# Kernel optimization log

Hardware: AMD Instinct MI355X
Metric: run time of the kernel (lower is better)

## Reference

```python
import jax, jax.numpy as jnp
import numpy as np

B, N, S, C1, C2 = 8, 8192, 2048, 128, 256
H1, H2 = 256, 256
EPS_LN = 1e-5


def _layernorm_c(x, g, b):
    # LayerNorm over channel dim of [B, C, N]
    mu = jnp.mean(x, axis=1, keepdims=True)
    var = jnp.mean((x - mu) ** 2, axis=1, keepdims=True)
    return g[None, :, None] * (x - mu) / jnp.sqrt(var + EPS_LN) + b[None, :, None]


def setup_inputs() -> dict:
    key = jax.random.key(0)
    ks = jax.random.split(key, 8)
    Cin = C1 + C2
    return {
        "points_coor1": jax.random.normal(ks[0], (B, 3, N), jnp.float32),
        "points_coor2": jax.random.normal(ks[1], (B, 3, S), jnp.float32),
        "points_fea1": jax.random.normal(ks[2], (B, C1, N), jnp.float32),
        "points_fea2": jax.random.normal(ks[3], (B, C2, S), jnp.float32),
        "points_padding2": jnp.zeros((B, S), dtype=bool),
        "W1": jax.random.normal(ks[4], (H1, Cin), jnp.float32) * 0.05,
        "b1": jnp.zeros((H1,), jnp.float32),
        "g1": jnp.ones((H1,), jnp.float32),
        "be1": jnp.zeros((H1,), jnp.float32),
        "W2": jax.random.normal(ks[5], (H2, H1), jnp.float32) * 0.05,
        "b2": jnp.zeros((H2,), jnp.float32),
        "g2": jnp.ones((H2,), jnp.float32),
        "be2": jnp.zeros((H2,), jnp.float32),
    }


def reference(points_coor1, points_coor2, points_fea1, points_fea2,
              points_padding2, W1, b1, g1, be1, W2, b2, g2, be2):
    c1 = jnp.transpose(points_coor1, (0, 2, 1))  # [B,N,3]
    c2 = jnp.transpose(points_coor2, (0, 2, 1))  # [B,S,3]
    f2 = jnp.transpose(points_fea2, (0, 2, 1))   # [B,S,C2]

    # push padded points far away (max computed on unmodified coords, as in torch RHS-first eval)
    big = jnp.max(jnp.abs(c2)) * 3.0
    c2 = jnp.where(points_padding2[..., None], big, c2)

    # squared euclidean pairwise distances [B,N,S]
    d = (jnp.sum(c1 * c1, -1)[:, :, None]
         + jnp.sum(c2 * c2, -1)[:, None, :]
         - 2.0 * jnp.einsum('bnd,bsd->bns', c1, c2))

    neg_d, idx = jax.lax.top_k(-d, 3)          # 3 smallest distances
    dists = -neg_d                              # [B,N,3]
    recip = 1.0 / jnp.clip(dists, 1e-8)
    w = recip / jnp.sum(recip, axis=-1, keepdims=True)  # [B,N,3]

    gathered = jax.vmap(lambda f, i: f[i])(f2, idx)     # [B,N,3,C2]
    interp = jnp.einsum('bnkc,bnk->bcn', gathered, w)   # [B,C2,N]

    x = jnp.concatenate([points_fea1, interp], axis=1)  # [B,C1+C2,N]
    x = jax.nn.relu(_layernorm_c(jnp.einsum('oc,bcn->bon', W1, x) + b1[None, :, None], g1, be1))
    x = jax.nn.relu(_layernorm_c(jnp.einsum('oc,bcn->bon', W2, x) + b2[None, :, None], g2, be2))
    return x
```

## Files before the change

### kernel.cpp

```cpp
#include <hip/hip_runtime.h>
#include <stdint.h>

#define BB 8
#define NPT 8192
#define SPT 2048
#define C1D 128
#define C2D 256
#define CIN 384
#define HD 256
#define SPLIT 8
#define SC (SPT/SPLIT)

typedef __attribute__((ext_vector_type(8))) short bf16x8;
typedef __attribute__((ext_vector_type(4))) float f32x4;

#define B2F(u) __uint_as_float(((unsigned int)(u)) << 16)

__device__ __forceinline__ unsigned short f2b(float f){
  unsigned int u = __float_as_uint(f);
  u += 0x7fffu + ((u >> 16) & 1u);
  return (unsigned short)(u >> 16);
}

__device__ __forceinline__ void bar_sync(){
  __builtin_amdgcn_sched_barrier(0);
  asm volatile("s_waitcnt lgkmcnt(0)" ::: "memory");
  __builtin_amdgcn_s_barrier();
  __builtin_amdgcn_sched_barrier(0);
}

__global__ __launch_bounds__(256) void gsrc_kernel(const float* __restrict__ coor2,
    const unsigned char* __restrict__ pad, float4* __restrict__ gs){
  int i = blockIdx.x * 256 + threadIdx.x;
  int b = i >> 11, s = i & (SPT - 1);
  const float* cb = coor2 + b * 3 * SPT;
  float x = cb[s], y = cb[SPT + s], z = cb[2*SPT + s];
  if (pad[i]) { x = 1e19f; y = 1e19f; z = 1e19f; }
  float n2 = __fadd_rn(__fadd_rn(__fmul_rn(x,x), __fmul_rn(y,y)), __fmul_rn(z,z));
  gs[i] = make_float4(x, y, z, n2);
}

#define NB_KNN 2048
#define NB_CVT 640
#define NB_T2 4096
#define NB_T1 8192
__global__ __launch_bounds__(256) void main_kernel(
    const float* __restrict__ coor1, const float4* __restrict__ gs,
    float* __restrict__ cv, int* __restrict__ cj,
    const float* __restrict__ W1, const float* __restrict__ W2, unsigned short* __restrict__ Wb,
    const float* __restrict__ fea2, unsigned short* __restrict__ f2t,
    const float* __restrict__ fea1, unsigned short* __restrict__ xpm){
  __shared__ unsigned short t[32][33];
  int bid = blockIdx.x, tid = threadIdx.x;
  if (bid < NB_KNN){
    int x = bid & 31, b = (bid >> 5) & 7, c = bid >> 8;
    int s0c = c * SC;
    const float4* gsb = gs + b * SPT + s0c;
    int n = x * 256 + tid;
    const float* ca = coor1 + b * 3 * NPT;
    float x1 = ca[n], y1 = ca[NPT + n], z1 = ca[2*NPT + n];
    float n1 = __fadd_rn(__fadd_rn(__fmul_rn(x1,x1), __fmul_rn(y1,y1)), __fmul_rn(z1,z1));
    float v0 = 3.4e38f, v1 = 3.4e38f, v2 = 3.4e38f;
    int j0 = 0, j1 = 0, j2 = 0;
    #pragma unroll 8
    for (int s = 0; s < SC; s++){
      float4 q = gsb[s];
      float dot = __fadd_rn(__fadd_rn(__fmul_rn(x1,q.x), __fmul_rn(y1,q.y)), __fmul_rn(z1,q.z));
      float npn = __fadd_rn(n1, q.w);
      float d = __builtin_fmaf(-2.0f, dot, npn);
      bool l0 = d < v0, l1 = d < v1, l2 = d < v2;
      j2 = l1 ? j1 : (l2 ? s : j2);
      j1 = l0 ? j0 : (l1 ? s : j1);
      j0 = l0 ? s  : j0;
      float nv2 = __builtin_amdgcn_fmed3f(v1, v2, d);
      float nv1 = __builtin_amdgcn_fmed3f(v0, v1, d);
      v0 = fminf(v0, d); v1 = nv1; v2 = nv2;
    }
    size_t m = (size_t)b * NPT + n;
    size_t base = (m * SPLIT + c) * 3;
    cv[base+0] = v0; cv[base+1] = v1; cv[base+2] = v2;
    cj[base+0] = s0c + j0; cj[base+1] = s0c + j1; cj[base+2] = s0c + j2;
    return;
  }
  bid -= NB_KNN;
  if (bid < NB_CVT){
    int i = bid * 256 + tid;
    const int n1 = HD * CIN;
    if (i < n1) Wb[i] = f2b(W1[i]);
    else { int k = i - n1; if (k < HD * HD) Wb[n1 + k] = f2b(W2[k]); }
    return;
  }
  bid -= NB_CVT;
  const float* src; unsigned short* dst; int Cdim, Ndim, dstStride, n0, c0, b;
  if (bid < NB_T2){
    src = fea2; dst = f2t; Cdim = C2D; Ndim = SPT; dstStride = C2D;
    n0 = (bid & 63) * 32; c0 = ((bid >> 6) & 7) * 32; b = bid >> 9;
  } else {
    bid -= NB_T2;
    src = fea1; dst = xpm; Cdim = C1D; Ndim = NPT; dstStride = CIN;
    n0 = (bid & 255) * 32; c0 = ((bid >> 8) & 3) * 32; b = bid >> 10;
  }
  int tx = tid & 31, ty = tid >> 5;
  const float* s = src + (size_t)b * Cdim * Ndim;
  unsigned short* d = dst + (size_t)b * Ndim * dstStride;
  #pragma unroll
  for (int i = 0; i < 4; i++)
    t[ty + i*8][tx] = f2b(s[(size_t)(c0 + ty + i*8) * Ndim + n0 + tx]);
  __syncthreads();
  #pragma unroll
  for (int i = 0; i < 4; i++)
    d[(size_t)(n0 + ty + i*8) * dstStride + c0 + tx] = t[tx][ty + i*8];
}

__global__ __launch_bounds__(256) void mlp_fused_kernel(
    const float* __restrict__ cv, const int* __restrict__ cj,
    const unsigned short* __restrict__ f2t, const unsigned short* __restrict__ xpm,
    const unsigned short* __restrict__ W1g, const unsigned short* __restrict__ W2g,
    const float* __restrict__ b1, const float* __restrict__ g1, const float* __restrict__ be1,
    const float* __restrict__ b2, const float* __restrict__ g2, const float* __restrict__ be2,
    float* __restrict__ outg){
  __shared__ __align__(16) unsigned short Ws[256*40];
  __shared__ __align__(16) unsigned short Hbuf[64*264];
  __shared__ __align__(16) unsigned short Xs[64*40];
  __shared__ float sB[256], sG[256], sBe[256];
  __shared__ float sW3[64*3];
  __shared__ int   sI3[64*3];
  int tid = threadIdx.x;
  int m0 = blockIdx.x * 64;
  int b = m0 >> 13, n0 = m0 & (NPT - 1);
  int w = tid >> 6, lane = tid & 63, col = lane & 15, quad = lane >> 4;
  int ml = w*16 + col;
  int mr = tid >> 2, part = tid & 3;
  const int4* wsrc  = (const int4*)(W1g + (size_t)tid * CIN);
  const int4* xsrc  = (const int4*)(xpm + (size_t)(m0 + mr) * CIN + part*8);
  int4 wA0 = wsrc[0], wA1 = wsrc[1], wA2 = wsrc[2], wA3 = wsrc[3];
  int4 xA  = xsrc[0];
  sB[tid] = b1[tid]; sG[tid] = g1[tid]; sBe[tid] = be1[tid];

  if (tid < 64){
    size_t m = (size_t)m0 + tid;
    float v0 = 3.4e38f, v1 = 3.4e38f, v2 = 3.4e38f;
    int j0 = 0, j1 = 0, j2 = 0;
    #pragma unroll
    for (int c = 0; c < SPLIT; c++){
      #pragma unroll
      for (int k = 0; k < 3; k++){
        float d = cv[(m * SPLIT + c) * 3 + k];
        int j   = cj[(m * SPLIT + c) * 3 + k];
        bool l0 = d < v0, l1 = d < v1, l2 = d < v2;
        j2 = l1 ? j1 : (l2 ? j : j2);
        j1 = l0 ? j0 : (l1 ? j : j1);
        j0 = l0 ? j  : j0;
        float nv2 = __builtin_amdgcn_fmed3f(v1, v2, d);
        float nv1 = __builtin_amdgcn_fmed3f(v0, v1, d);
        v0 = fminf(v0, d); v1 = nv1; v2 = nv2;
      }
    }
    float r0 = 1.0f / fmaxf(v0, 1e-8f);
    float r1 = 1.0f / fmaxf(v1, 1e-8f);
    float r2 = 1.0f / fmaxf(v2, 1e-8f);
    float rs = (r0 + r1) + r2;
    sW3[tid*3+0] = r0 / rs; sW3[tid*3+1] = r1 / rs; sW3[tid*3+2] = r2 / rs;
    sI3[tid*3+0] = j0; sI3[tid*3+1] = j1; sI3[tid*3+2] = j2;
  }
  bar_sync();

  {
    int pbase = w*16;
    #pragma unroll 4
    for (int i = 0; i < 16; i++){
      int p = pbase + i;
      float w0 = sW3[p*3+0], w1 = sW3[p*3+1], w2 = sW3[p*3+2];
      int j0 = sI3[p*3+0], j1 = sI3[p*3+1], j2 = sI3[p*3+2];
      const ushort4 a  = *(const ushort4*)(f2t + (size_t)(b*SPT + j0) * C2D + lane*4);
      const ushort4 c4 = *(const ushort4*)(f2t + (size_t)(b*SPT + j1) * C2D + lane*4);
      const ushort4 e  = *(const ushort4*)(f2t + (size_t)(b*SPT + j2) * C2D + lane*4);
      ushort4 o;
      o.x = f2b(w0*B2F(a.x) + w1*B2F(c4.x) + w2*B2F(e.x));
      o.y = f2b(w0*B2F(a.y) + w1*B2F(c4.y) + w2*B2F(e.y));
      o.z = f2b(w0*B2F(a.z) + w1*B2F(c4.z) + w2*B2F(e.z));
      o.w = f2b(w0*B2F(a.w) + w1*B2F(c4.w) + w2*B2F(e.w));
      *(ushort4*)(Hbuf + p*264 + lane*4) = o;
    }
  }
  f32x4 acc[16];
  #pragma unroll
  for (int i = 0; i < 16; i++) acc[i] = (f32x4)0.0f;

  for (int c = 0; c < 12; c++){
    bar_sync();
    {
      int4* d4 = (int4*)(Ws + tid * 40);
      d4[0] = wA0; d4[1] = wA1; d4[2] = wA2; d4[3] = wA3;
      if (c < 4) *(int4*)(Xs + mr*40 + part*8) = xA;
    }
    if (c + 1 < 12){
      wA0 = wsrc[(c+1)*4 + 0]; wA1 = wsrc[(c+1)*4 + 1];
      wA2 = wsrc[(c+1)*4 + 2]; wA3 = wsrc[(c+1)*4 + 3];
      if (c + 1 < 4) xA = xsrc[(c+1)*4];
    }
    bar_sync();
    bf16x8 bfrag = (c < 4)
      ? *(const bf16x8*)(Xs + ml*40 + quad*8)
      : *(const bf16x8*)(Hbuf + ml*264 + (c-4)*32 + quad*8);
    #pragma unroll
    for (int ot = 0; ot < 16; ot++){
      bf16x8 afrag = *(const bf16x8*)(Ws + (ot*16 + col)*40 + quad*8);
      acc[ot] = __builtin_amdgcn_mfma_f32_16x16x32_bf16(afrag, bfrag, acc[ot], 0, 0, 0);
    }
  }
  const int4* w2src = (const int4*)(W2g + (size_t)tid * HD);
  int4 v0r = w2src[0], v1r = w2src[1], v2r = w2src[2], v3r = w2src[3];
  float rb2 = b2[tid], rg2 = g2[tid], rbe2 = be2[tid];
  {
    float s1 = 0.f, s2 = 0.f;
    #pragma unroll
    for (int ot = 0; ot < 16; ot++)
      #pragma unroll
      for (int r = 0; r < 4; r++){
        int o = ot*16 + quad*4 + r;
        float v = acc[ot][r] + sB[o];
        acc[ot][r] = v;
        s1 += v; s2 += v*v;
      }
    s1 += __shfl_xor(s1, 16); s1 += __shfl_xor(s1, 32);
    s2 += __shfl_xor(s2, 16); s2 += __shfl_xor(s2, 32);
    float mu = s1 * (1.f/256.f);
    float rinv = rsqrtf(s2 * (1.f/256.f) - mu*mu + 1e-5f);
    bar_sync();
    #pragma unroll
    for (int ot = 0; ot < 16; ot++){
      int ob = ot*16 + quad*4;
      ushort4 hv;
      hv.x = f2b(fmaxf((acc[ot][0] - mu) * rinv * sG[ob+0] + sBe[ob+0], 0.f));
      hv.y = f2b(fmaxf((acc[ot][1] - mu) * rinv * sG[ob+1] + sBe[ob+1], 0.f));
      hv.z = f2b(fmaxf((acc[ot][2] - mu) * rinv * sG[ob+2] + sBe[ob+2], 0.f));
      hv.w = f2b(fmaxf((acc[ot][3] - mu) * rinv * sG[ob+3] + sBe[ob+3], 0.f));
      *(ushort4*)(Hbuf + ml*264 + ot*16 + quad*4) = hv;
    }
  }
  bar_sync();
  sB[tid] = rb2; sG[tid] = rg2; sBe[tid] = rbe2;

  #pragma unroll
  for (int i = 0; i < 16; i++) acc[i] = (f32x4)0.0f;
  for (int c = 0; c < 8; c++){
    bar_sync();
    {
      int4* d4 = (int4*)(Ws + tid * 40);
      d4[0] = v0r; d4[1] = v1r; d4[2] = v2r; d4[3] = v3r;
    }
    if (c + 1 < 8){
      v0r = w2src[(c+1)*4 + 0]; v1r = w2src[(c+1)*4 + 1];
      v2r = w2src[(c+1)*4 + 2]; v3r = w2src[(c+1)*4 + 3];
    }
    bar_sync();
    bf16x8 bfrag = *(const bf16x8*)(Hbuf + ml*264 + c*32 + quad*8);
    #pragma unroll
    for (int ot = 0; ot < 16; ot++){
      bf16x8 afrag = *(const bf16x8*)(Ws + (ot*16 + col)*40 + quad*8);
      acc[ot] = __builtin_amdgcn_mfma_f32_16x16x32_bf16(afrag, bfrag, acc[ot], 0, 0, 0);
    }
  }
  float s1 = 0.f, s2 = 0.f;
  #pragma unroll
  for (int ot = 0; ot < 16; ot++)
    #pragma unroll
    for (int r = 0; r < 4; r++){
      int o = ot*16 + quad*4 + r;
      float v = acc[ot][r] + sB[o];
      acc[ot][r] = v;
      s1 += v; s2 += v*v;
    }
  s1 += __shfl_xor(s1, 16); s1 += __shfl_xor(s1, 32);
  s2 += __shfl_xor(s2, 16); s2 += __shfl_xor(s2, 32);
  float mu = s1 * (1.f/256.f);
  float rinv = rsqrtf(s2 * (1.f/256.f) - mu*mu + 1e-5f);
  size_t obase = (size_t)b * HD * NPT + n0 + w*16 + col;
  #pragma unroll
  for (int ot = 0; ot < 16; ot++)
    #pragma unroll
    for (int r = 0; r < 4; r++){
      int o = ot*16 + quad*4 + r;
      float v = (acc[ot][r] - mu) * rinv * sG[o] + sBe[o];
      outg[obase + (size_t)o * NPT] = fmaxf(v, 0.f);
    }
}

extern "C" void kernel_launch(void* const* d_in, const int* in_sizes, int n_in,
                              void* d_out, int out_size, void* d_ws, size_t ws_size,
                              hipStream_t stream){
  const float* coor1 = (const float*)d_in[0];
  const float* coor2 = (const float*)d_in[1];
  const float* fea1  = (const float*)d_in[2];
  const float* fea2  = (const float*)d_in[3];
  const unsigned char* pad = (const unsigned char*)d_in[4];
  const float* W1  = (const float*)d_in[5];
  const float* b1  = (const float*)d_in[6];
  const float* g1  = (const float*)d_in[7];
  const float* be1 = (const float*)d_in[8];
  const float* W2  = (const float*)d_in[9];
  const float* b2  = (const float*)d_in[10];
  const float* g2  = (const float*)d_in[11];
  const float* be2 = (const float*)d_in[12];
  float* out = (float*)d_out;

  char* ws = (char*)d_ws;
  unsigned short* W1b  = (unsigned short*)(ws + 1573120);
  unsigned short* W2b  = (unsigned short*)(ws + 1769728);
  unsigned short* f2t  = (unsigned short*)(ws + 1900800);
  unsigned short* xpm  = (unsigned short*)(ws + 10289408);
  float* cv            = (float*)(ws + 60621056);
  int*   cj            = (int*)  (ws + 60621056 + 6291456);
  float4* gs           = (float4*)(ws + 60621056 + 16777216);

  gsrc_kernel<<<BB*SPT/256, 256, 0, stream>>>(coor2, pad, gs);
  main_kernel<<<NB_KNN + NB_CVT + NB_T2 + NB_T1, 256, 0, stream>>>(
      coor1, gs, cv, cj, W1, W2, W1b, fea2, f2t, fea1, xpm);
  mlp_fused_kernel<<<BB*NPT/64, 256, 0, stream>>>(
      cv, cj, f2t, xpm, W1b, W2b, b1, g1, be1, b2, g2, be2, out);
}
```

Baseline: 233.1 us.

## Drop LDS weight staging and block barriers in fused MLP kernel

The fused MLP kernel no longer stages W1/W2 and the input-feature tile through shared memory behind block-wide barriers. Each wave now reads its MFMA A and B fragments straight from global memory, relying on L2/L1 for reuse. The three-NN weights and indices pass between lanes by shuffle instead of LDS, and the bias/gamma/beta vectors are read as float4 from global. This removes most barriers and shrinks LDS use, which may raise occupancy, but each wave issues many more global loads for the weights, which now depend on cache hits.

```diff
diff --git a/kernel.cpp b/kernel.cpp
--- a/kernel.cpp
+++ b/kernel.cpp
@@ -20,13 +20,6 @@
   unsigned int u = __float_as_uint(f);
   u += 0x7fffu + ((u >> 16) & 1u);
   return (unsigned short)(u >> 16);
-}
-
-__device__ __forceinline__ void bar_sync(){
-  __builtin_amdgcn_sched_barrier(0);
-  asm volatile("s_waitcnt lgkmcnt(0)" ::: "memory");
-  __builtin_amdgcn_s_barrier();
-  __builtin_amdgcn_sched_barrier(0);
 }
 
 __global__ __launch_bounds__(256) void gsrc_kernel(const float* __restrict__ coor2,
@@ -119,26 +112,17 @@
     const float* __restrict__ b1, const float* __restrict__ g1, const float* __restrict__ be1,
     const float* __restrict__ b2, const float* __restrict__ g2, const float* __restrict__ be2,
     float* __restrict__ outg){
-  __shared__ __align__(16) unsigned short Ws[256*40];
   __shared__ __align__(16) unsigned short Hbuf[64*264];
-  __shared__ __align__(16) unsigned short Xs[64*40];
-  __shared__ float sB[256], sG[256], sBe[256];
-  __shared__ float sW3[64*3];
-  __shared__ int   sI3[64*3];
   int tid = threadIdx.x;
   int m0 = blockIdx.x * 64;
   int b = m0 >> 13, n0 = m0 & (NPT - 1);
   int w = tid >> 6, lane = tid & 63, col = lane & 15, quad = lane >> 4;
   int ml = w*16 + col;
-  int mr = tid >> 2, part = tid & 3;
-  const int4* wsrc  = (const int4*)(W1g + (size_t)tid * CIN);
-  const int4* xsrc  = (const int4*)(xpm + (size_t)(m0 + mr) * CIN + part*8);
-  int4 wA0 = wsrc[0], wA1 = wsrc[1], wA2 = wsrc[2], wA3 = wsrc[3];
-  int4 xA  = xsrc[0];
-  sB[tid] = b1[tid]; sG[tid] = g1[tid]; sBe[tid] = be1[tid];
-
-  if (tid < 64){
-    size_t m = (size_t)m0 + tid;
+
+  float w0r = 0.f, w1r = 0.f, w2r = 0.f;
+  int j0r = 0, j1r = 0, j2r = 0;
+  if (lane < 16){
+    size_t m = (size_t)m0 + w*16 + lane;
     float v0 = 3.4e38f, v1 = 3.4e38f, v2 = 3.4e38f;
     int j0 = 0, j1 = 0, j2 = 0;
     #pragma unroll
@@ -160,131 +144,115 @@
     float r1 = 1.0f / fmaxf(v1, 1e-8f);
     float r2 = 1.0f / fmaxf(v2, 1e-8f);
     float rs = (r0 + r1) + r2;
-    sW3[tid*3+0] = r0 / rs; sW3[tid*3+1] = r1 / rs; sW3[tid*3+2] = r2 / rs;
-    sI3[tid*3+0] = j0; sI3[tid*3+1] = j1; sI3[tid*3+2] = j2;
-  }
-  bar_sync();
-
+    w0r = r0 / rs; w1r = r1 / rs; w2r = r2 / rs;
+    j0r = j0; j1r = j1; j2r = j2;
+  }
+
+  #pragma unroll 4
+  for (int i = 0; i < 16; i++){
+    float w0 = __shfl(w0r, i), w1 = __shfl(w1r, i), w2 = __shfl(w2r, i);
+    int j0 = __shfl(j0r, i), j1 = __shfl(j1r, i), j2 = __shfl(j2r, i);
+    const ushort4 a  = *(const ushort4*)(f2t + (size_t)(b*SPT + j0) * C2D + lane*4);
+    const ushort4 c4 = *(const ushort4*)(f2t + (size_t)(b*SPT + j1) * C2D + lane*4);
+    const ushort4 e  = *(const ushort4*)(f2t + (size_t)(b*SPT + j2) * C2D + lane*4);
+    ushort4 o;
+    o.x = f2b(w0*B2F(a.x) + w1*B2F(c4.x) + w2*B2F(e.x));
+    o.y = f2b(w0*B2F(a.y) + w1*B2F(c4.y) + w2*B2F(e.y));
+    o.z = f2b(w0*B2F(a.z) + w1*B2F(c4.z) + w2*B2F(e.z));
+    o.w = f2b(w0*B2F(a.w) + w1*B2F(c4.w) + w2*B2F(e.w));
+    *(ushort4*)(Hbuf + (w*16 + i)*264 + lane*4) = o;
+  }
+
+  f32x4 acc[16];
+  #pragma unroll
+  for (int i = 0; i < 16; i++) acc[i] = (f32x4)0.0f;
+
+  const unsigned short* xrow = xpm + (size_t)(m0 + ml) * CIN + quad*8;
+  for (int c = 0; c < 12; c++){
+    bf16x8 bfrag = (c < 4)
+      ? *(const bf16x8*)(xrow + c*32)
+      : *(const bf16x8*)(Hbuf + ml*264 + (c-4)*32 + quad*8);
+    #pragma unroll
+    for (int ot = 0; ot < 16; ot++){
+      bf16x8 afrag = *(const bf16x8*)(W1g + (size_t)(ot*16 + col) * CIN + c*32 + quad*8);
+      acc[ot] = __builtin_amdgcn_mfma_f32_16x16x32_bf16(afrag, bfrag, acc[ot], 0, 0, 0);
+    }
+  }
   {
-    int pbase = w*16;
-    #pragma unroll 4
-    for (int i = 0; i < 16; i++){
-      int p = pbase + i;
-      float w0 = sW3[p*3+0], w1 = sW3[p*3+1], w2 = sW3[p*3+2];
-      int j0 = sI3[p*3+0], j1 = sI3[p*3+1], j2 = sI3[p*3+2];
-      const ushort4 a  = *(const ushort4*)(f2t + (size_t)(b*SPT + j0) * C2D + lane*4);
-      const ushort4 c4 = *(const ushort4*)(f2t + (size_t)(b*SPT + j1) * C2D + lane*4);
-      const ushort4 e  = *(const ushort4*)(f2t + (size_t)(b*SPT + j2) * C2D + lane*4);
-      ushort4 o;
-      o.x = f2b(w0*B2F(a.x) + w1*B2F(c4.x) + w2*B2F(e.x));
-      o.y = f2b(w0*B2F(a.y) + w1*B2F(c4.y) + w2*B2F(e.y));
-      o.z = f2b(w0*B2F(a.z) + w1*B2F(c4.z) + w2*B2F(e.z));
-      o.w = f2b(w0*B2F(a.w) + w1*B2F(c4.w) + w2*B2F(e.w));
-      *(ushort4*)(Hbuf + p*264 + lane*4) = o;
-    }
-  }
-  f32x4 acc[16];
-  #pragma unroll
-  for (int i = 0; i < 16; i++) acc[i] = (f32x4)0.0f;
-
-  for (int c = 0; c < 12; c++){
-    bar_sync();
-    {
-      int4* d4 = (int4*)(Ws + tid * 40);
-      d4[0] = wA0; d4[1] = wA1; d4[2] = wA2; d4[3] = wA3;
-      if (c < 4) *(int4*)(Xs + mr*40 + part*8) = xA;
-    }
-    if (c + 1 < 12){
-      wA0 = wsrc[(c+1)*4 + 0]; wA1 = wsrc[(c+1)*4 + 1];
-      wA2 = wsrc[(c+1)*4 + 2]; wA3 = wsrc[(c+1)*4 + 3];
-      if (c + 1 < 4) xA = xsrc[(c+1)*4];
-    }
-    bar_sync();
-    bf16x8 bfrag = (c < 4)
-      ? *(const bf16x8*)(Xs + ml*40 + quad*8)
-      : *(const bf16x8*)(Hbuf + ml*264 + (c-4)*32 + quad*8);
-    #pragma unroll
-    for (int ot = 0; ot < 16; ot++){
-      bf16x8 afrag = *(const bf16x8*)(Ws + (ot*16 + col)*40 + quad*8);
-      acc[ot] = __builtin_amdgcn_mfma_f32_16x16x32_bf16(afrag, bfrag, acc[ot], 0, 0, 0);
-    }
-  }
-  const int4* w2src = (const int4*)(W2g + (size_t)tid * HD);
-  int4 v0r = w2src[0], v1r = w2src[1], v2r = w2src[2], v3r = w2src[3];
-  float rb2 = b2[tid], rg2 = g2[tid], rbe2 = be2[tid];
-  {
+    const float4* b1v = (const float4*)b1;
+    const float4* g1v = (const float4*)g1;
+    const float4* be1v = (const float4*)be1;
     float s1 = 0.f, s2 = 0.f;
     #pragma unroll
-    for (int ot = 0; ot < 16; ot++)
-      #pragma unroll
-      for (int r = 0; r < 4; r++){
-        int o = ot*16 + quad*4 + r;
-        float v = acc[ot][r] + sB[o];
-        acc[ot][r] = v;
-        s1 += v; s2 += v*v;
-      }
+    for (int ot = 0; ot < 16; ot++){
+      float4 bb = b1v[ot*4 + quad];
+      float v0a = acc[ot][0] + bb.x, v1a = acc[ot][1] + bb.y;
+      float v2a = acc[ot][2] + bb.z, v3a = acc[ot][3] + bb.w;
+      acc[ot][0] = v0a; acc[ot][1] = v1a; acc[ot][2] = v2a; acc[ot][3] = v3a;
+      s1 += v0a; s2 += v0a*v0a; s1 += v1a; s2 += v1a*v1a;
+      s1 += v2a; s2 += v2a*v2a; s1 += v3a; s2 += v3a*v3a;
+    }
     s1 += __shfl_xor(s1, 16); s1 += __shfl_xor(s1, 32);
     s2 += __shfl_xor(s2, 16); s2 += __shfl_xor(s2, 32);
     float mu = s1 * (1.f/256.f);
     float rinv = rsqrtf(s2 * (1.f/256.f) - mu*mu + 1e-5f);
-    bar_sync();
-    #pragma unroll
-    for (int ot = 0; ot < 16; ot++){
-      int ob = ot*16 + quad*4;
+    #pragma unroll
+    for (int ot = 0; ot < 16; ot++){
+      float4 gg = g1v[ot*4 + quad];
+      float4 ee = be1v[ot*4 + quad];
       ushort4 hv;
-      hv.x = f2b(fmaxf((acc[ot][0] - mu) * rinv * sG[ob+0] + sBe[ob+0], 0.f));
-      hv.y = f2b(fmaxf((acc[ot][1] - mu) * rinv * sG[ob+1] + sBe[ob+1], 0.f));
-      hv.z = f2b(fmaxf((acc[ot][2] - mu) * rinv * sG[ob+2] + sBe[ob+2], 0.f));
-      hv.w = f2b(fmaxf((acc[ot][3] - mu) * rinv * sG[ob+3] + sBe[ob+3], 0.f));
+      hv.x = f2b(fmaxf((acc[ot][0] - mu) * rinv * gg.x + ee.x, 0.f));
+      hv.y = f2b(fmaxf((acc[ot][1] - mu) * rinv * gg.y + ee.y, 0.f));
+      hv.z = f2b(fmaxf((acc[ot][2] - mu) * rinv * gg.z + ee.z, 0.f));
+      hv.w = f2b(fmaxf((acc[ot][3] - mu) * rinv * gg.w + ee.w, 0.f));
       *(ushort4*)(Hbuf + ml*264 + ot*16 + quad*4) = hv;
     }
   }
-  bar_sync();
-  sB[tid] = rb2; sG[tid] = rg2; sBe[tid] = rbe2;
 
   #pragma unroll
   for (int i = 0; i < 16; i++) acc[i] = (f32x4)0.0f;
   for (int c = 0; c < 8; c++){
-    bar_sync();
-    {
-      int4* d4 = (int4*)(Ws + tid * 40);
-      d4[0] = v0r; d4[1] = v1r; d4[2] = v2r; d4[3] = v3r;
-    }
-    if (c + 1 < 8){
-      v0r = w2src[(c+1)*4 + 0]; v1r = w2src[(c+1)*4 + 1];
-      v2r = w2src[(c+1)*4 + 2]; v3r = w2src[(c+1)*4 + 3];
-    }
-    bar_sync();
     bf16x8 bfrag = *(const bf16x8*)(Hbuf + ml*264 + c*32 + quad*8);
     #pragma unroll
     for (int ot = 0; ot < 16; ot++){
-      bf16x8 afrag = *(const bf16x8*)(Ws + (ot*16 + col)*40 + quad*8);
+      bf16x8 afrag = *(const bf16x8*)(W2g + (size_t)(ot*16 + col) * HD + c*32 + quad*8);
       acc[ot] = __builtin_amdgcn_mfma_f32_16x16x32_bf16(afrag, bfrag, acc[ot], 0, 0, 0);
     }
   }
-  float s1 = 0.f, s2 = 0.f;
-  #pragma unroll
-  for (int ot = 0; ot < 16; ot++)
-    #pragma unroll
-    for (int r = 0; r < 4; r++){
-      int o = ot*16 + quad*4 + r;
-      float v = acc[ot][r] + sB[o];
-      acc[ot][r] = v;
-      s1 += v; s2 += v*v;
-    }
-  s1 += __shfl_xor(s1, 16); s1 += __shfl_xor(s1, 32);
-  s2 += __shfl_xor(s2, 16); s2 += __shfl_xor(s2, 32);
-  float mu = s1 * (1.f/256.f);
-  float rinv = rsqrtf(s2 * (1.f/256.f) - mu*mu + 1e-5f);
-  size_t obase = (size_t)b * HD * NPT + n0 + w*16 + col;
-  #pragma unroll
-  for (int ot = 0; ot < 16; ot++)
-    #pragma unroll
-    for (int r = 0; r < 4; r++){
-      int o = ot*16 + quad*4 + r;
-      float v = (acc[ot][r] - mu) * rinv * sG[o] + sBe[o];
-      outg[obase + (size_t)o * NPT] = fmaxf(v, 0.f);
-    }
+  {
+    const float4* b2v = (const float4*)b2;
+    const float4* g2v = (const float4*)g2;
+    const float4* be2v = (const float4*)be2;
+    float s1 = 0.f, s2 = 0.f;
+    #pragma unroll
+    for (int ot = 0; ot < 16; ot++){
+      float4 bb = b2v[ot*4 + quad];
+      float v0a = acc[ot][0] + bb.x, v1a = acc[ot][1] + bb.y;
+      float v2a = acc[ot][2] + bb.z, v3a = acc[ot][3] + bb.w;
+      acc[ot][0] = v0a; acc[ot][1] = v1a; acc[ot][2] = v2a; acc[ot][3] = v3a;
+      s1 += v0a; s2 += v0a*v0a; s1 += v1a; s2 += v1a*v1a;
+      s1 += v2a; s2 += v2a*v2a; s1 += v3a; s2 += v3a*v3a;
+    }
+    s1 += __shfl_xor(s1, 16); s1 += __shfl_xor(s1, 32);
+    s2 += __shfl_xor(s2, 16); s2 += __shfl_xor(s2, 32);
+    float mu = s1 * (1.f/256.f);
+    float rinv = rsqrtf(s2 * (1.f/256.f) - mu*mu + 1e-5f);
+    size_t obase = (size_t)b * HD * NPT + n0 + w*16 + col;
+    #pragma unroll
+    for (int ot = 0; ot < 16; ot++){
+      float4 gg = g2v[ot*4 + quad];
+      float4 ee = be2v[ot*4 + quad];
+      float o0 = fmaxf((acc[ot][0] - mu) * rinv * gg.x + ee.x, 0.f);
+      float o1 = fmaxf((acc[ot][1] - mu) * rinv * gg.y + ee.y, 0.f);
+      float o2 = fmaxf((acc[ot][2] - mu) * rinv * gg.z + ee.z, 0.f);
+      float o3 = fmaxf((acc[ot][3] - mu) * rinv * gg.w + ee.w, 0.f);
+      int ob = ot*16 + quad*4;
+      outg[obase + (size_t)(ob+0) * NPT] = o0;
+      outg[obase + (size_t)(ob+1) * NPT] = o1;
+      outg[obase + (size_t)(ob+2) * NPT] = o2;
+      outg[obase + (size_t)(ob+3) * NPT] = o3;
+    }
+  }
 }
 
 extern "C" void kernel_launch(void* const* d_in, const int* in_sizes, int n_in,
```

Result: slower. 373.8 us (+60.3%).

## Double K-chunk per barrier, load X directly to registers, shuffle interp weights

Applied to the files above, without the earlier changes.

The weight staging chunk grows from 32 to 64 K-columns, which halves the number of barrier-separated iterations in both MLP GEMMs. The fea1 operand is now loaded straight into MFMA fragment registers instead of being staged through shared memory. The top-3 weights and indices are broadcast within each wave with shuffles rather than through shared arrays and a barrier. Two barriers around the LayerNorm writeback are also dropped. The cost is more registers (8+4 int4 prefetch), more LDS for the weights, and a risk of races on Hbuf and sB now that those barriers are gone.

```diff
diff --git a/kernel.cpp b/kernel.cpp
--- a/kernel.cpp
+++ b/kernel.cpp
@@ -119,26 +119,28 @@
     const float* __restrict__ b1, const float* __restrict__ g1, const float* __restrict__ be1,
     const float* __restrict__ b2, const float* __restrict__ g2, const float* __restrict__ be2,
     float* __restrict__ outg){
-  __shared__ __align__(16) unsigned short Ws[256*40];
+  __shared__ __align__(16) unsigned short Ws[256*72];
   __shared__ __align__(16) unsigned short Hbuf[64*264];
-  __shared__ __align__(16) unsigned short Xs[64*40];
   __shared__ float sB[256], sG[256], sBe[256];
-  __shared__ float sW3[64*3];
-  __shared__ int   sI3[64*3];
   int tid = threadIdx.x;
   int m0 = blockIdx.x * 64;
   int b = m0 >> 13, n0 = m0 & (NPT - 1);
   int w = tid >> 6, lane = tid & 63, col = lane & 15, quad = lane >> 4;
   int ml = w*16 + col;
-  int mr = tid >> 2, part = tid & 3;
-  const int4* wsrc  = (const int4*)(W1g + (size_t)tid * CIN);
-  const int4* xsrc  = (const int4*)(xpm + (size_t)(m0 + mr) * CIN + part*8);
-  int4 wA0 = wsrc[0], wA1 = wsrc[1], wA2 = wsrc[2], wA3 = wsrc[3];
-  int4 xA  = xsrc[0];
+  const int4* wsrc = (const int4*)(W1g + (size_t)tid * CIN);
+  int4 wA[8];
+  #pragma unroll
+  for (int i = 0; i < 8; i++) wA[i] = wsrc[i];
+  const unsigned short* xrow = xpm + (size_t)(m0 + ml) * CIN + quad*8;
+  bf16x8 xA[4];
+  #pragma unroll
+  for (int i = 0; i < 4; i++) xA[i] = *(const bf16x8*)(xrow + i*32);
   sB[tid] = b1[tid]; sG[tid] = g1[tid]; sBe[tid] = be1[tid];
 
-  if (tid < 64){
-    size_t m = (size_t)m0 + tid;
+  float w0r = 0.f, w1r = 0.f, w2r = 0.f;
+  int j0r = 0, j1r = 0, j2r = 0;
+  if (lane < 16){
+    size_t m = (size_t)m0 + w*16 + lane;
     float v0 = 3.4e38f, v1 = 3.4e38f, v2 = 3.4e38f;
     int j0 = 0, j1 = 0, j2 = 0;
     #pragma unroll
@@ -160,57 +162,58 @@
     float r1 = 1.0f / fmaxf(v1, 1e-8f);
     float r2 = 1.0f / fmaxf(v2, 1e-8f);
     float rs = (r0 + r1) + r2;
-    sW3[tid*3+0] = r0 / rs; sW3[tid*3+1] = r1 / rs; sW3[tid*3+2] = r2 / rs;
-    sI3[tid*3+0] = j0; sI3[tid*3+1] = j1; sI3[tid*3+2] = j2;
-  }
-  bar_sync();
-
-  {
-    int pbase = w*16;
-    #pragma unroll 4
-    for (int i = 0; i < 16; i++){
-      int p = pbase + i;
-      float w0 = sW3[p*3+0], w1 = sW3[p*3+1], w2 = sW3[p*3+2];
-      int j0 = sI3[p*3+0], j1 = sI3[p*3+1], j2 = sI3[p*3+2];
-      const ushort4 a  = *(const ushort4*)(f2t + (size_t)(b*SPT + j0) * C2D + lane*4);
-      const ushort4 c4 = *(const ushort4*)(f2t + (size_t)(b*SPT + j1) * C2D + lane*4);
-      const ushort4 e  = *(const ushort4*)(f2t + (size_t)(b*SPT + j2) * C2D + lane*4);
-      ushort4 o;
-      o.x = f2b(w0*B2F(a.x) + w1*B2F(c4.x) + w2*B2F(e.x));
-      o.y = f2b(w0*B2F(a.y) + w1*B2F(c4.y) + w2*B2F(e.y));
-      o.z = f2b(w0*B2F(a.z) + w1*B2F(c4.z) + w2*B2F(e.z));
-      o.w = f2b(w0*B2F(a.w) + w1*B2F(c4.w) + w2*B2F(e.w));
-      *(ushort4*)(Hbuf + p*264 + lane*4) = o;
-    }
-  }
+    w0r = r0 / rs; w1r = r1 / rs; w2r = r2 / rs;
+    j0r = j0; j1r = j1; j2r = j2;
+  }
+
+  #pragma unroll 4
+  for (int i = 0; i < 16; i++){
+    float w0 = __shfl(w0r, i), w1 = __shfl(w1r, i), w2 = __shfl(w2r, i);
+    int j0 = __shfl(j0r, i), j1 = __shfl(j1r, i), j2 = __shfl(j2r, i);
+    const ushort4 a  = *(const ushort4*)(f2t + (size_t)(b*SPT + j0) * C2D + lane*4);
+    const ushort4 c4 = *(const ushort4*)(f2t + (size_t)(b*SPT + j1) * C2D + lane*4);
+    const ushort4 e  = *(const ushort4*)(f2t + (size_t)(b*SPT + j2) * C2D + lane*4);
+    ushort4 o;
+    o.x = f2b(w0*B2F(a.x) + w1*B2F(c4.x) + w2*B2F(e.x));
+    o.y = f2b(w0*B2F(a.y) + w1*B2F(c4.y) + w2*B2F(e.y));
+    o.z = f2b(w0*B2F(a.z) + w1*B2F(c4.z) + w2*B2F(e.z));
+    o.w = f2b(w0*B2F(a.w) + w1*B2F(c4.w) + w2*B2F(e.w));
+    *(ushort4*)(Hbuf + (w*16 + i)*264 + lane*4) = o;
+  }
+
   f32x4 acc[16];
   #pragma unroll
   for (int i = 0; i < 16; i++) acc[i] = (f32x4)0.0f;
 
-  for (int c = 0; c < 12; c++){
+  for (int c = 0; c < 6; c++){
     bar_sync();
     {
-      int4* d4 = (int4*)(Ws + tid * 40);
-      d4[0] = wA0; d4[1] = wA1; d4[2] = wA2; d4[3] = wA3;
-      if (c < 4) *(int4*)(Xs + mr*40 + part*8) = xA;
-    }
-    if (c + 1 < 12){
-      wA0 = wsrc[(c+1)*4 + 0]; wA1 = wsrc[(c+1)*4 + 1];
-      wA2 = wsrc[(c+1)*4 + 2]; wA3 = wsrc[(c+1)*4 + 3];
-      if (c + 1 < 4) xA = xsrc[(c+1)*4];
+      int4* d4 = (int4*)(Ws + tid * 72);
+      #pragma unroll
+      for (int i = 0; i < 8; i++) d4[i] = wA[i];
+    }
+    if (c + 1 < 6){
+      #pragma unroll
+      for (int i = 0; i < 8; i++) wA[i] = wsrc[(c+1)*8 + i];
     }
     bar_sync();
-    bf16x8 bfrag = (c < 4)
-      ? *(const bf16x8*)(Xs + ml*40 + quad*8)
-      : *(const bf16x8*)(Hbuf + ml*264 + (c-4)*32 + quad*8);
-    #pragma unroll
-    for (int ot = 0; ot < 16; ot++){
-      bf16x8 afrag = *(const bf16x8*)(Ws + (ot*16 + col)*40 + quad*8);
-      acc[ot] = __builtin_amdgcn_mfma_f32_16x16x32_bf16(afrag, bfrag, acc[ot], 0, 0, 0);
+    #pragma unroll
+    for (int ks = 0; ks < 2; ks++){
+      int kc = c*2 + ks;
+      bf16x8 bfrag = (kc < 4)
+        ? xA[kc]
+        : *(const bf16x8*)(Hbuf + ml*264 + (kc-4)*32 + quad*8);
+      #pragma unroll
+      for (int ot = 0; ot < 16; ot++){
+        bf16x8 afrag = *(const bf16x8*)(Ws + (ot*16 + col)*72 + ks*32 + quad*8);
+        acc[ot] = __builtin_amdgcn_mfma_f32_16x16x32_bf16(afrag, bfrag, acc[ot], 0, 0, 0);
+      }
     }
   }
   const int4* w2src = (const int4*)(W2g + (size_t)tid * HD);
-  int4 v0r = w2src[0], v1r = w2src[1], v2r = w2src[2], v3r = w2src[3];
+  int4 wB[8];
+  #pragma unroll
+  for (int i = 0; i < 8; i++) wB[i] = w2src[i];
   float rb2 = b2[tid], rg2 = g2[tid], rbe2 = be2[tid];
   {
     float s1 = 0.f, s2 = 0.f;
@@ -227,7 +230,6 @@
     s2 += __shfl_xor(s2, 16); s2 += __shfl_xor(s2, 32);
     float mu = s1 * (1.f/256.f);
     float rinv = rsqrtf(s2 * (1.f/256.f) - mu*mu + 1e-5f);
-    bar_sync();
     #pragma unroll
     for (int ot = 0; ot < 16; ot++){
       int ob = ot*16 + quad*4;
@@ -239,27 +241,30 @@
       *(ushort4*)(Hbuf + ml*264 + ot*16 + quad*4) = hv;
     }
   }
-  bar_sync();
-  sB[tid] = rb2; sG[tid] = rg2; sBe[tid] = rbe2;
 
   #pragma unroll
   for (int i = 0; i < 16; i++) acc[i] = (f32x4)0.0f;
-  for (int c = 0; c < 8; c++){
+  for (int c = 0; c < 4; c++){
     bar_sync();
     {
-      int4* d4 = (int4*)(Ws + tid * 40);
-      d4[0] = v0r; d4[1] = v1r; d4[2] = v2r; d4[3] = v3r;
-    }
-    if (c + 1 < 8){
-      v0r = w2src[(c+1)*4 + 0]; v1r = w2src[(c+1)*4 + 1];
-      v2r = w2src[(c+1)*4 + 2]; v3r = w2src[(c+1)*4 + 3];
+      int4* d4 = (int4*)(Ws + tid * 72);
+      #pragma unroll
+      for (int i = 0; i < 8; i++) d4[i] = wB[i];
+    }
+    if (c == 0){ sB[tid] = rb2; sG[tid] = rg2; sBe[tid] = rbe2; }
+    if (c + 1 < 4){
+      #pragma unroll
+      for (int i = 0; i < 8; i++) wB[i] = w2src[(c+1)*8 + i];
     }
     bar_sync();
-    bf16x8 bfrag = *(const bf16x8*)(Hbuf + ml*264 + c*32 + quad*8);
-    #pragma unroll
-    for (int ot = 0; ot < 16; ot++){
-      bf16x8 afrag = *(const bf16x8*)(Ws + (ot*16 + col)*40 + quad*8);
-      acc[ot] = __builtin_amdgcn_mfma_f32_16x16x32_bf16(afrag, bfrag, acc[ot], 0, 0, 0);
+    #pragma unroll
+    for (int ks = 0; ks < 2; ks++){
+      bf16x8 bfrag = *(const bf16x8*)(Hbuf + ml*264 + (c*2+ks)*32 + quad*8);
+      #pragma unroll
+      for (int ot = 0; ot < 16; ot++){
+        bf16x8 afrag = *(const bf16x8*)(Ws + (ot*16 + col)*72 + ks*32 + quad*8);
+        acc[ot] = __builtin_amdgcn_mfma_f32_16x16x32_bf16(afrag, bfrag, acc[ot], 0, 0, 0);
+      }
     }
   }
   float s1 = 0.f, s2 = 0.f;
```

Result: slower. 300.8 us (+29.0%).
